# Performance work log

Measured on AMD Instinct MI355X. Metric: run time of the kernel, lower is better.

## Reference

```python
import jax, jax.numpy as jnp
import numpy as np

HIDDEN = 2048
N_HEADS = 32
N_KV_HEADS = 8
HEAD_DIM = HIDDEN // N_HEADS  # 64
N_REP = N_HEADS // N_KV_HEADS  # 4
ROPE_THETA = 10000.0


def setup_inputs() -> dict:
    key = jax.random.key(0)
    ks = jax.random.split(key, 5)
    b, s = 2, 2048
    x = jax.random.normal(ks[0], (b, s, HIDDEN), dtype=jnp.float32)
    position_ids = jnp.arange(b * s, dtype=jnp.int32).reshape(b, s)
    sc = 1.0 / np.sqrt(HIDDEN)
    Wq = jax.random.normal(ks[1], (HIDDEN, HIDDEN), dtype=jnp.float32) * sc
    Wk = jax.random.normal(ks[2], (HIDDEN, N_KV_HEADS * HEAD_DIM), dtype=jnp.float32) * sc
    Wv = jax.random.normal(ks[3], (HIDDEN, N_KV_HEADS * HEAD_DIM), dtype=jnp.float32) * sc
    Wo = jax.random.normal(ks[4], (HIDDEN, HIDDEN), dtype=jnp.float32) * sc
    return {"input_ids": x, "Wq": Wq, "Wk": Wk, "Wv": Wv, "Wo": Wo,
            "position_ids": position_ids}


def _rope_cos_sin(position_ids, dtype):
    # inv_freq: [head_dim/2]
    inv_freq = 1.0 / (ROPE_THETA ** (jnp.arange(0, HEAD_DIM, 2, dtype=jnp.float32) / HEAD_DIM))
    freqs = position_ids.astype(jnp.float32)[..., None] * inv_freq  # [b, s, d/2]
    emb = jnp.concatenate([freqs, freqs], axis=-1)  # [b, s, d]
    return emb.astype(dtype), None  # placeholder, replaced below


def _rotate_half(x):
    x1, x2 = jnp.split(x, 2, axis=-1)
    return jnp.concatenate([-x2, x1], axis=-1)


def reference(input_ids, Wq, Wk, Wv, Wo, position_ids):
    b, s, _ = input_ids.shape
    q = (input_ids @ Wq).reshape(b, s, N_HEADS, HEAD_DIM).transpose(0, 2, 1, 3)      # [b,H,s,d]
    k = (input_ids @ Wk).reshape(b, s, N_KV_HEADS, HEAD_DIM).transpose(0, 2, 1, 3)   # [b,Hkv,s,d]
    v = (input_ids @ Wv).reshape(b, s, N_KV_HEADS, HEAD_DIM).transpose(0, 2, 1, 3)

    # RoPE
    inv_freq = 1.0 / (ROPE_THETA ** (jnp.arange(0, HEAD_DIM, 2, dtype=jnp.float32) / HEAD_DIM))
    freqs = position_ids.astype(jnp.float32)[..., None] * inv_freq  # [b,s,d/2]
    emb = jnp.concatenate([freqs, freqs], axis=-1)                   # [b,s,d]
    cos = jnp.cos(emb).astype(input_ids.dtype)[:, None, :, :]        # [b,1,s,d]
    sin = jnp.sin(emb).astype(input_ids.dtype)[:, None, :, :]
    q = q * cos + _rotate_half(q) * sin
    k = k * cos + _rotate_half(k) * sin

    # repeat_kv: [b,Hkv,s,d] -> [b,H,s,d]
    k = jnp.repeat(k, N_REP, axis=1)
    v = jnp.repeat(v, N_REP, axis=1)

    # causal SDPA
    scale = 1.0 / np.sqrt(HEAD_DIM)
    scores = jnp.einsum('bhqd,bhkd->bhqk', q, k) * scale
    causal = jnp.tril(jnp.ones((s, s), dtype=bool))
    scores = jnp.where(causal, scores, jnp.finfo(scores.dtype).min)
    attn = jax.nn.softmax(scores, axis=-1)
    out = jnp.einsum('bhqk,bhkd->bhqd', attn, v)                     # [b,H,s,d]
    out = out.transpose(0, 2, 1, 3).reshape(b, s, HIDDEN)
    return out @ Wo
```

## Files before the change

kernel.cpp:

```cpp
#include <hip/hip_runtime.h>
#include <hip/hip_bf16.h>

#define HIDDEN 2048
#define NHEADS 32
#define NKVH   8
#define HD     64
#define BATCH  2
#define SEQ    2048
#define ROWS   (BATCH * SEQ)
#define NQKV   3072
#define KCOL   2048
#define VCOL   2560

typedef __bf16 bf16x8 __attribute__((ext_vector_type(8)));
typedef __bf16 bf16x4 __attribute__((ext_vector_type(4)));
typedef float  f32x4  __attribute__((ext_vector_type(4)));
typedef short  s16x4  __attribute__((ext_vector_type(4)));
typedef short  s16x8  __attribute__((ext_vector_type(8)));

__device__ __forceinline__ void gl2lds16(const void* g, void* l) {
  __builtin_amdgcn_global_load_lds(
      (const __attribute__((address_space(1))) void*)g,
      (__attribute__((address_space(3))) void*)l, 16, 0, 0);
}

__device__ __forceinline__ short f2bs(float f) {
  __bf16 h = (__bf16)f;
  return __builtin_bit_cast(short, h);
}

__device__ __forceinline__ f32x4 mfma16(s16x4 a, s16x4 b, f32x4 c) {
#if __has_builtin(__builtin_amdgcn_mfma_f32_16x16x16bf16_1k)
  return __builtin_amdgcn_mfma_f32_16x16x16bf16_1k(a, b, c, 0, 0, 0);
#else
  s16x8 z = {0,0,0,0,0,0,0,0};
  s16x8 a8 = __builtin_shufflevector(a, (s16x4){0,0,0,0}, 0,1,2,3,4,5,6,7);
  s16x8 b8 = __builtin_shufflevector(b, (s16x4){0,0,0,0}, 0,1,2,3,4,5,6,7);
  a8[4]=0;a8[5]=0;a8[6]=0;a8[7]=0; b8[4]=0;b8[5]=0;b8[6]=0;b8[7]=0;
  return __builtin_amdgcn_mfma_f32_16x16x32_bf16(
      __builtin_bit_cast(bf16x8, a8), __builtin_bit_cast(bf16x8, b8), c, 0, 0, 0);
#endif
}

__global__ void convert_bf16(const float* __restrict__ src, __bf16* __restrict__ dst,
                             int n8) {
  int i = blockIdx.x * blockDim.x + threadIdx.x;
  if (i >= n8) return;
  const float4* s = (const float4*)(src + (size_t)i * 8);
  float4 a = s[0], b = s[1];
  bf16x8 o;
  o[0] = (__bf16)a.x; o[1] = (__bf16)a.y; o[2] = (__bf16)a.z; o[3] = (__bf16)a.w;
  o[4] = (__bf16)b.x; o[5] = (__bf16)b.y; o[6] = (__bf16)b.z; o[7] = (__bf16)b.w;
  *(bf16x8*)(dst + (size_t)i * 8) = o;
}

__global__ void wtrans(const float* __restrict__ Wq, const float* __restrict__ Wk,
                       const float* __restrict__ Wv, const float* __restrict__ Wo,
                       __bf16* __restrict__ dst) {
  __shared__ __bf16 tile[32][33];
  int n0 = blockIdx.x * 32, k0 = blockIdx.y * 32;
  int tx = threadIdx.x, ty = threadIdx.y;
  const float* src;
  int N, c0;
  if (n0 < 2048)      { src = Wq; N = 2048; c0 = n0; }
  else if (n0 < 2560) { src = Wk; N = 512;  c0 = n0 - 2048; }
  else if (n0 < 3072) { src = Wv; N = 512;  c0 = n0 - 2560; }
  else                { src = Wo; N = 2048; c0 = n0 - 3072; }
#pragma unroll
  for (int i = 0; i < 32; i += 8)
    tile[ty + i][tx] = (__bf16)src[(size_t)(k0 + ty + i) * N + (c0 + tx)];
  __syncthreads();
#pragma unroll
  for (int i = 0; i < 32; i += 8)
    dst[(size_t)(n0 + ty + i) * HIDDEN + (k0 + tx)] = tile[tx][ty + i];
}

template <typename OutT, bool ROPE>
__launch_bounds__(256, 2)
__global__ void gemm_bt(const __bf16* __restrict__ A, const __bf16* __restrict__ Bt,
                        OutT* __restrict__ C, int M, int N, int K,
                        const int* __restrict__ pos_ids, __bf16* __restrict__ Vt) {
  __shared__ __bf16 As[128 * 32];
  __shared__ __bf16 Bs[128 * 32];
  int bn = blockIdx.x, bm = blockIdx.y;
  int t = threadIdx.x;
  int wave = t >> 6, lane = t & 63, l16 = lane & 15, quad = lane >> 4;
  int wm = (wave >> 1) * 64, wn = (wave & 1) * 64;

  f32x4 acc[4][4] = {};

  int arow = t >> 2;
  int ac   = (t & 3) * 8;
  const __bf16* Ag = A  + (size_t)(bm * 128 + arow) * K + ac;
  const __bf16* Bg = Bt + (size_t)(bn * 128 + arow) * K + ac;
  __bf16* AsW0 = As + wave * 512;
  __bf16* AsW1 = As + 2048 + wave * 512;
  __bf16* BsW0 = Bs + wave * 512;
  __bf16* BsW1 = Bs + 2048 + wave * 512;

  for (int k0 = 0; k0 < K; k0 += 32) {
    __syncthreads();
    gl2lds16(Ag + k0, AsW0);
    gl2lds16(Ag + (size_t)64 * K + k0, AsW1);
    gl2lds16(Bg + k0, BsW0);
    gl2lds16(Bg + (size_t)64 * K + k0, BsW1);
    __syncthreads();

    bf16x8 af[4], bfr[4];
#pragma unroll
    for (int i = 0; i < 4; ++i) {
      af[i]  = *(const bf16x8*)(&As[(wm + i * 16 + l16) * 32 + quad * 8]);
      bfr[i] = *(const bf16x8*)(&Bs[(wn + i * 16 + l16) * 32 + quad * 8]);
    }
#pragma unroll
    for (int i = 0; i < 4; ++i)
#pragma unroll
      for (int j = 0; j < 4; ++j)
        acc[i][j] = __builtin_amdgcn_mfma_f32_16x16x32_bf16(af[i], bfr[j], acc[i][j], 0, 0, 0);
  }

  if (ROPE) {
    int headidx = bn * 2 + (wn >> 6);
    if (headidx >= 40) {
#pragma unroll
      for (int i = 0; i < 4; ++i) {
        int srow = bm * 128 + wm + i * 16 + quad * 4;
        int b = srow >> 11, s = srow & 2047;
#pragma unroll
        for (int j = 0; j < 4; ++j) {
          int vcol = bn * 128 + wn + j * 16 + l16 - VCOL;
          int hk = vcol >> 6, d = vcol & 63;
          bf16x4 w;
#pragma unroll
          for (int r = 0; r < 4; ++r) w[r] = (__bf16)acc[i][j][r];
          *(bf16x4*)(Vt + ((size_t)(b * NKVH + hk) * HD + d) * SEQ + s) = w;
        }
      }
      return;
    }
    float invrev0 = __expf(-(float)l16 * 0.28782313662425574f) * 0.15915494309189535f;
    float invrev1 = __expf(-(float)(l16 + 16) * 0.28782313662425574f) * 0.15915494309189535f;
#pragma unroll
    for (int i = 0; i < 4; ++i)
#pragma unroll
      for (int r = 0; r < 4; ++r) {
        int gr = bm * 128 + wm + i * 16 + quad * 4 + r;
        float pos = (float)pos_ids[gr];
        float rv0 = pos * invrev0; rv0 -= floorf(rv0);
        float rv1 = pos * invrev1; rv1 -= floorf(rv1);
        float a0 = rv0 * 6.283185307179586f, a1 = rv1 * 6.283185307179586f;
        float s0 = __sinf(a0), c0 = __cosf(a0);
        float s1 = __sinf(a1), c1 = __cosf(a1);
        float x0 = acc[i][0][r], x2 = acc[i][2][r];
        acc[i][0][r] = x0 * c0 - x2 * s0;
        acc[i][2][r] = x2 * c0 + x0 * s0;
        float x1 = acc[i][1][r], x3 = acc[i][3][r];
        acc[i][1][r] = x1 * c1 - x3 * s1;
        acc[i][3][r] = x3 * c1 + x1 * s1;
      }
  }

#pragma unroll
  for (int i = 0; i < 4; ++i)
#pragma unroll
    for (int j = 0; j < 4; ++j)
#pragma unroll
      for (int r = 0; r < 4; ++r)
        C[(size_t)(bm * 128 + wm + i * 16 + quad * 4 + r) * N +
          (bn * 128 + wn + j * 16 + l16)] = (OutT)acc[i][j][r];
}

__launch_bounds__(256, 3)
__global__ void flash_attn(const __bf16* __restrict__ QKV, const __bf16* __restrict__ Vt,
                           __bf16* __restrict__ O) {
  int p = blockIdx.x >> 1, h2 = blockIdx.x & 1;
  int hk = blockIdx.y, b = blockIdx.z;
  int t = threadIdx.x;
  int wave = t >> 6, lane = t & 63, l16 = lane & 15, quad = lane >> 4;
  int hh = h2 * 2 + (wave >> 1);
  int h  = hk * 4 + hh;
  int qs = wave & 1;

  __shared__ __bf16 Ks[2][2][64 * 32];
  __shared__ __bf16 Vs[2][4096];

  const __bf16* Kbase = QKV + (size_t)(b * SEQ) * NQKV + KCOL + hk * HD;
  const __bf16* VtB   = Vt + (size_t)(b * NKVH + hk) * HD * SEQ;

  int kr = wave * 16 + (lane >> 2);
  int kc = (lane & 3) * 8;
  int vd = wave * 16 + (lane >> 2);
  int vsc = (lane & 3) * 16;
  int vs4w = (lane & 3) * 4;

  for (int seg = 0; seg < 2; ++seg) {
    int qt = seg ? (31 - p) : p;

    __syncthreads();

    bf16x8 qfrag[2][2];
#pragma unroll
    for (int qi = 0; qi < 2; ++qi) {
      const __bf16* qp = QKV + (size_t)(b * SEQ + qt * 64 + qs * 32 + qi * 16 + l16) * NQKV
                       + h * HD + quad * 8;
      bf16x8 q0 = *(const bf16x8*)qp;
      bf16x8 q1 = *(const bf16x8*)(qp + 32);
#pragma unroll
      for (int e = 0; e < 8; ++e) {
        qfrag[qi][0][e] = (__bf16)((float)q0[e] * 0.125f);
        qfrag[qi][1][e] = (__bf16)((float)q1[e] * 0.125f);
      }
    }

    float lsum[2] = {0.f, 0.f};
    f32x4 oacc[2][4];
#pragma unroll
    for (int qi = 0; qi < 2; ++qi)
#pragma unroll
      for (int dt = 0; dt < 4; ++dt) oacc[qi][dt] = (f32x4){0.f, 0.f, 0.f, 0.f};

    {
      const __bf16* kp = Kbase + (size_t)kr * NQKV + kc;
      gl2lds16(kp,      &Ks[0][0][wave * 512]);
      gl2lds16(kp + 32, &Ks[0][1][wave * 512]);
      const __bf16* vp = VtB + (size_t)vd * SEQ + vsc;
      s16x8 v0 = __builtin_bit_cast(s16x8, *(const bf16x8*)vp);
      s16x8 v1 = __builtin_bit_cast(s16x8, *(const bf16x8*)(vp + 8));
      *(s16x4*)(&Vs[0][(vs4w + 0) * 256 + vd * 4]) = __builtin_shufflevector(v0, v0, 0, 1, 2, 3);
      *(s16x4*)(&Vs[0][(vs4w + 1) * 256 + vd * 4]) = __builtin_shufflevector(v0, v0, 4, 5, 6, 7);
      *(s16x4*)(&Vs[0][(vs4w + 2) * 256 + vd * 4]) = __builtin_shufflevector(v1, v1, 0, 1, 2, 3);
      *(s16x4*)(&Vs[0][(vs4w + 3) * 256 + vd * 4]) = __builtin_shufflevector(v1, v1, 4, 5, 6, 7);
    }

    for (int kt = 0; kt <= qt; ++kt) {
      int buf = kt & 1;
      __syncthreads();

      bool pre = (kt < qt);
      s16x8 pv0, pv1;
      if (pre) {
        const __bf16* kp = Kbase + (size_t)((kt + 1) * 64 + kr) * NQKV + kc;
        gl2lds16(kp,      &Ks[buf ^ 1][0][wave * 512]);
        gl2lds16(kp + 32, &Ks[buf ^ 1][1][wave * 512]);
        const __bf16* vp = VtB + (size_t)vd * SEQ + (kt + 1) * 64 + vsc;
        pv0 = __builtin_bit_cast(s16x8, *(const bf16x8*)vp);
        pv1 = __builtin_bit_cast(s16x8, *(const bf16x8*)(vp + 8));
      }

      f32x4 sacc[2][4];
#pragma unroll
      for (int qi = 0; qi < 2; ++qi)
#pragma unroll
        for (int nt = 0; nt < 4; ++nt) sacc[qi][nt] = (f32x4){0.f, 0.f, 0.f, 0.f};
#pragma unroll
      for (int ks = 0; ks < 2; ++ks) {
        bf16x8 kf[4];
#pragma unroll
        for (int nt = 0; nt < 4; ++nt)
          kf[nt] = *(const bf16x8*)(&Ks[buf][ks][(nt * 16 + l16) * 32 + quad * 8]);
#pragma unroll
        for (int nt = 0; nt < 4; ++nt)
#pragma unroll
          for (int qi = 0; qi < 2; ++qi)
            sacc[qi][nt] = __builtin_amdgcn_mfma_f32_16x16x32_bf16(kf[nt], qfrag[qi][ks], sacc[qi][nt], 0, 0, 0);
      }

      s16x4 af[2][4];
      if (kt == qt) {
#pragma unroll
        for (int qi = 0; qi < 2; ++qi)
#pragma unroll
          for (int nt = 0; nt < 4; ++nt)
#pragma unroll
            for (int r = 0; r < 4; ++r) {
              int kg = nt * 16 + quad * 4 + r;
              int qg = qs * 32 + qi * 16 + l16;
              float e = __expf((kg > qg) ? -1e30f : sacc[qi][nt][r]);
              lsum[qi] += e;
              af[qi][nt][r] = f2bs(e);
            }
      } else {
#pragma unroll
        for (int qi = 0; qi < 2; ++qi)
#pragma unroll
          for (int nt = 0; nt < 4; ++nt)
#pragma unroll
            for (int r = 0; r < 4; ++r) {
              float e = __expf(sacc[qi][nt][r]);
              lsum[qi] += e;
              af[qi][nt][r] = f2bs(e);
            }
      }

#pragma unroll
      for (int nt = 0; nt < 4; ++nt) {
        s16x4 vf[4];
#pragma unroll
        for (int dt = 0; dt < 4; ++dt)
          vf[dt] = *(const s16x4*)(&Vs[buf][(nt * 4 + quad) * 256 + (dt * 16 + l16) * 4]);
#pragma unroll
        for (int qi = 0; qi < 2; ++qi)
#pragma unroll
          for (int dt = 0; dt < 4; ++dt)
            oacc[qi][dt] = mfma16(af[qi][nt], vf[dt], oacc[qi][dt]);
      }

      if (pre) {
        *(s16x4*)(&Vs[buf ^ 1][(vs4w + 0) * 256 + vd * 4]) = __builtin_shufflevector(pv0, pv0, 0, 1, 2, 3);
        *(s16x4*)(&Vs[buf ^ 1][(vs4w + 1) * 256 + vd * 4]) = __builtin_shufflevector(pv0, pv0, 4, 5, 6, 7);
        *(s16x4*)(&Vs[buf ^ 1][(vs4w + 2) * 256 + vd * 4]) = __builtin_shufflevector(pv1, pv1, 0, 1, 2, 3);
        *(s16x4*)(&Vs[buf ^ 1][(vs4w + 3) * 256 + vd * 4]) = __builtin_shufflevector(pv1, pv1, 4, 5, 6, 7);
      }
    }

#pragma unroll
    for (int qi = 0; qi < 2; ++qi) {
      float l = lsum[qi];
      l += __shfl_xor(l, 16);
      l += __shfl_xor(l, 32);
#pragma unroll
      for (int r = 0; r < 4; ++r) {
        float lr = __shfl(l, quad * 4 + r);
        float inv = 1.0f / lr;
#pragma unroll
        for (int dt = 0; dt < 4; ++dt) {
          float o = oacc[qi][dt][r] * inv;
          O[(size_t)(b * SEQ + qt * 64 + qs * 32 + qi * 16 + quad * 4 + r) * HIDDEN +
            h * HD + dt * 16 + l16] = (__bf16)o;
        }
      }
    }
  }
}

extern "C" void kernel_launch(void* const* d_in, const int* in_sizes, int n_in,
                              void* d_out, int out_size, void* d_ws, size_t ws_size,
                              hipStream_t stream) {
  const float* x  = (const float*)d_in[0];
  const float* Wq = (const float*)d_in[1];
  const float* Wk = (const float*)d_in[2];
  const float* Wv = (const float*)d_in[3];
  const float* Wo = (const float*)d_in[4];
  const int* pos  = (const int*)d_in[5];

  __bf16* Wqkvt = (__bf16*)d_ws;
  __bf16* Wot   = Wqkvt + (size_t)NQKV * HIDDEN;
  __bf16* Xb    = Wot + (size_t)HIDDEN * HIDDEN;
  __bf16* QKV   = Xb + (size_t)ROWS * HIDDEN;
  __bf16* Oat   = QKV + (size_t)ROWS * NQKV;
  __bf16* Vt    = Xb;

  wtrans<<<dim3(160, 64), dim3(32, 8), 0, stream>>>(Wq, Wk, Wv, Wo, Wqkvt);
  convert_bf16<<<(ROWS * HIDDEN / 8 + 255) / 256, 256, 0, stream>>>(x, Xb, ROWS * HIDDEN / 8);

  gemm_bt<__bf16, true><<<dim3(NQKV / 128, ROWS / 128), 256, 0, stream>>>(
      Xb, Wqkvt, QKV, ROWS, NQKV, HIDDEN, pos, Vt);

  flash_attn<<<dim3(32, NKVH, BATCH), 256, 0, stream>>>(QKV, Vt, Oat);

  gemm_bt<float, false><<<dim3(HIDDEN / 128, ROWS / 128), 256, 0, stream>>>(
      Oat, Wot, (float*)d_out, ROWS, HIDDEN, HIDDEN, nullptr, nullptr);
}
```

Measured before the change: 287.7 us.

## Merge prep kernels, deepen GEMM k-step, and swizzle GEMM block order

The weight-transpose and input-conversion kernels are merged into one launch, which saves a kernel launch. The GEMM now loads a 64-wide k slab per barrier pair into two LDS buffers and runs two MFMA sub-steps, halving the number of syncs per K. Blocks are remapped from a 1D id so groups of neighbouring M tiles share the same N tile, aiming for better L2 reuse. LDS use doubles, which may lower occupancy.

```diff
diff --git a/kernel.cpp b/kernel.cpp
--- a/kernel.cpp
+++ b/kernel.cpp
@@ -33,7 +33,6 @@
 #if __has_builtin(__builtin_amdgcn_mfma_f32_16x16x16bf16_1k)
   return __builtin_amdgcn_mfma_f32_16x16x16bf16_1k(a, b, c, 0, 0, 0);
 #else
-  s16x8 z = {0,0,0,0,0,0,0,0};
   s16x8 a8 = __builtin_shufflevector(a, (s16x4){0,0,0,0}, 0,1,2,3,4,5,6,7);
   s16x8 b8 = __builtin_shufflevector(b, (s16x4){0,0,0,0}, 0,1,2,3,4,5,6,7);
   a8[4]=0;a8[5]=0;a8[6]=0;a8[7]=0; b8[4]=0;b8[5]=0;b8[6]=0;b8[7]=0;
@@ -42,37 +41,40 @@
 #endif
 }
 
-__global__ void convert_bf16(const float* __restrict__ src, __bf16* __restrict__ dst,
-                             int n8) {
-  int i = blockIdx.x * blockDim.x + threadIdx.x;
-  if (i >= n8) return;
-  const float4* s = (const float4*)(src + (size_t)i * 8);
-  float4 a = s[0], b = s[1];
-  bf16x8 o;
-  o[0] = (__bf16)a.x; o[1] = (__bf16)a.y; o[2] = (__bf16)a.z; o[3] = (__bf16)a.w;
-  o[4] = (__bf16)b.x; o[5] = (__bf16)b.y; o[6] = (__bf16)b.z; o[7] = (__bf16)b.w;
-  *(bf16x8*)(dst + (size_t)i * 8) = o;
-}
-
-__global__ void wtrans(const float* __restrict__ Wq, const float* __restrict__ Wk,
-                       const float* __restrict__ Wv, const float* __restrict__ Wo,
-                       __bf16* __restrict__ dst) {
+__global__ void prep(const float* __restrict__ Wq, const float* __restrict__ Wk,
+                     const float* __restrict__ Wv, const float* __restrict__ Wo,
+                     const float* __restrict__ x,
+                     __bf16* __restrict__ dstW, __bf16* __restrict__ Xb) {
   __shared__ __bf16 tile[32][33];
-  int n0 = blockIdx.x * 32, k0 = blockIdx.y * 32;
-  int tx = threadIdx.x, ty = threadIdx.y;
-  const float* src;
-  int N, c0;
-  if (n0 < 2048)      { src = Wq; N = 2048; c0 = n0; }
-  else if (n0 < 2560) { src = Wk; N = 512;  c0 = n0 - 2048; }
-  else if (n0 < 3072) { src = Wv; N = 512;  c0 = n0 - 2560; }
-  else                { src = Wo; N = 2048; c0 = n0 - 3072; }
-#pragma unroll
-  for (int i = 0; i < 32; i += 8)
-    tile[ty + i][tx] = (__bf16)src[(size_t)(k0 + ty + i) * N + (c0 + tx)];
-  __syncthreads();
-#pragma unroll
-  for (int i = 0; i < 32; i += 8)
-    dst[(size_t)(n0 + ty + i) * HIDDEN + (k0 + tx)] = tile[tx][ty + i];
+  int bid = blockIdx.x, tid = threadIdx.x;
+  if (bid < 10240) {
+    int n0 = (bid % 160) * 32, k0 = (bid / 160) * 32;
+    int tx = tid & 31, ty = tid >> 5;
+    const float* src;
+    int N, c0;
+    if (n0 < 2048)      { src = Wq; N = 2048; c0 = n0; }
+    else if (n0 < 2560) { src = Wk; N = 512;  c0 = n0 - 2048; }
+    else if (n0 < 3072) { src = Wv; N = 512;  c0 = n0 - 2560; }
+    else                { src = Wo; N = 2048; c0 = n0 - 3072; }
+#pragma unroll
+    for (int i = 0; i < 32; i += 8)
+      tile[ty + i][tx] = (__bf16)src[(size_t)(k0 + ty + i) * N + (c0 + tx)];
+    __syncthreads();
+#pragma unroll
+    for (int i = 0; i < 32; i += 8)
+      dstW[(size_t)(n0 + ty + i) * HIDDEN + (k0 + tx)] = tile[tx][ty + i];
+  } else {
+    size_t i = (size_t)(bid - 10240) * 256 + tid;
+    const float4* s = (const float4*)(x + i * 16);
+    float4 a = s[0], b = s[1], c = s[2], d = s[3];
+    bf16x8 o0, o1;
+    o0[0] = (__bf16)a.x; o0[1] = (__bf16)a.y; o0[2] = (__bf16)a.z; o0[3] = (__bf16)a.w;
+    o0[4] = (__bf16)b.x; o0[5] = (__bf16)b.y; o0[6] = (__bf16)b.z; o0[7] = (__bf16)b.w;
+    o1[0] = (__bf16)c.x; o1[1] = (__bf16)c.y; o1[2] = (__bf16)c.z; o1[3] = (__bf16)c.w;
+    o1[4] = (__bf16)d.x; o1[5] = (__bf16)d.y; o1[6] = (__bf16)d.z; o1[7] = (__bf16)d.w;
+    *(bf16x8*)(Xb + i * 16)     = o0;
+    *(bf16x8*)(Xb + i * 16 + 8) = o1;
+  }
 }
 
 template <typename OutT, bool ROPE>
@@ -80,9 +82,11 @@
 __global__ void gemm_bt(const __bf16* __restrict__ A, const __bf16* __restrict__ Bt,
                         OutT* __restrict__ C, int M, int N, int K,
                         const int* __restrict__ pos_ids, __bf16* __restrict__ Vt) {
-  __shared__ __bf16 As[128 * 32];
-  __shared__ __bf16 Bs[128 * 32];
-  int bn = blockIdx.x, bm = blockIdx.y;
+  __shared__ __bf16 As[2][128 * 32];
+  __shared__ __bf16 Bs[2][128 * 32];
+  int id = blockIdx.x;
+  int bm = (id & 7) * 4 + ((id >> 3) & 3);
+  int bn = id >> 5;
   int t = threadIdx.x;
   int wave = t >> 6, lane = t & 63, l16 = lane & 15, quad = lane >> 4;
   int wm = (wave >> 1) * 64, wn = (wave & 1) * 64;
@@ -93,30 +97,34 @@
   int ac   = (t & 3) * 8;
   const __bf16* Ag = A  + (size_t)(bm * 128 + arow) * K + ac;
   const __bf16* Bg = Bt + (size_t)(bn * 128 + arow) * K + ac;
-  __bf16* AsW0 = As + wave * 512;
-  __bf16* AsW1 = As + 2048 + wave * 512;
-  __bf16* BsW0 = Bs + wave * 512;
-  __bf16* BsW1 = Bs + 2048 + wave * 512;
-
-  for (int k0 = 0; k0 < K; k0 += 32) {
+  int woff = wave * 512;
+
+  for (int k0 = 0; k0 < K; k0 += 64) {
     __syncthreads();
-    gl2lds16(Ag + k0, AsW0);
-    gl2lds16(Ag + (size_t)64 * K + k0, AsW1);
-    gl2lds16(Bg + k0, BsW0);
-    gl2lds16(Bg + (size_t)64 * K + k0, BsW1);
+    gl2lds16(Ag + k0,                      &As[0][woff]);
+    gl2lds16(Ag + (size_t)64 * K + k0,      &As[0][2048 + woff]);
+    gl2lds16(Ag + k0 + 32,                 &As[1][woff]);
+    gl2lds16(Ag + (size_t)64 * K + k0 + 32, &As[1][2048 + woff]);
+    gl2lds16(Bg + k0,                      &Bs[0][woff]);
+    gl2lds16(Bg + (size_t)64 * K + k0,      &Bs[0][2048 + woff]);
+    gl2lds16(Bg + k0 + 32,                 &Bs[1][woff]);
+    gl2lds16(Bg + (size_t)64 * K + k0 + 32, &Bs[1][2048 + woff]);
     __syncthreads();
 
-    bf16x8 af[4], bfr[4];
-#pragma unroll
-    for (int i = 0; i < 4; ++i) {
-      af[i]  = *(const bf16x8*)(&As[(wm + i * 16 + l16) * 32 + quad * 8]);
-      bfr[i] = *(const bf16x8*)(&Bs[(wn + i * 16 + l16) * 32 + quad * 8]);
-    }
-#pragma unroll
-    for (int i = 0; i < 4; ++i)
-#pragma unroll
-      for (int j = 0; j < 4; ++j)
-        acc[i][j] = __builtin_amdgcn_mfma_f32_16x16x32_bf16(af[i], bfr[j], acc[i][j], 0, 0, 0);
+#pragma unroll
+    for (int ks = 0; ks < 2; ++ks) {
+      bf16x8 af[4], bfr[4];
+#pragma unroll
+      for (int i = 0; i < 4; ++i) {
+        af[i]  = *(const bf16x8*)(&As[ks][(wm + i * 16 + l16) * 32 + quad * 8]);
+        bfr[i] = *(const bf16x8*)(&Bs[ks][(wn + i * 16 + l16) * 32 + quad * 8]);
+      }
+#pragma unroll
+      for (int i = 0; i < 4; ++i)
+#pragma unroll
+        for (int j = 0; j < 4; ++j)
+          acc[i][j] = __builtin_amdgcn_mfma_f32_16x16x32_bf16(af[i], bfr[j], acc[i][j], 0, 0, 0);
+    }
   }
 
   if (ROPE) {
@@ -350,14 +358,13 @@
   __bf16* Oat   = QKV + (size_t)ROWS * NQKV;
   __bf16* Vt    = Xb;
 
-  wtrans<<<dim3(160, 64), dim3(32, 8), 0, stream>>>(Wq, Wk, Wv, Wo, Wqkvt);
-  convert_bf16<<<(ROWS * HIDDEN / 8 + 255) / 256, 256, 0, stream>>>(x, Xb, ROWS * HIDDEN / 8);
-
-  gemm_bt<__bf16, true><<<dim3(NQKV / 128, ROWS / 128), 256, 0, stream>>>(
+  prep<<<dim3(12288), 256, 0, stream>>>(Wq, Wk, Wv, Wo, x, Wqkvt, Xb);
+
+  gemm_bt<__bf16, true><<<dim3(768), 256, 0, stream>>>(
       Xb, Wqkvt, QKV, ROWS, NQKV, HIDDEN, pos, Vt);
 
   flash_attn<<<dim3(32, NKVH, BATCH), 256, 0, stream>>>(QKV, Vt, Oat);
 
-  gemm_bt<float, false><<<dim3(HIDDEN / 128, ROWS / 128), 256, 0, stream>>>(
+  gemm_bt<float, false><<<dim3(512), 256, 0, stream>>>(
       Oat, Wot, (float*)d_out, ROWS, HIDDEN, HIDDEN, nullptr, nullptr);
 }
```

Measured after the change: 268.8 us. -6.6%, faster.
